# Optimization experiments

Measured on AMD Instinct MI355X. Metric: run time of the kernel, lower is better.

## Reference

```python
import jax, jax.numpy as jnp
import numpy as np

N_NODES = 100000
N_EDGES = 200000
B = 256        # batch of query (center) nodes
K = 20         # n_neighbors
D = 128        # node feature dim
TD = 128       # time encoding dim
IMP = 100      # importance_dim
DK = 256       # attention key dim
H = 4 * (D + TD)  # LSTM hidden per init_para_for_one_depth = 1024
FEAT = D + D + TD + IMP  # 484: [neigh_x, edge_x, edge_tx, neigh_imp]


def setup_inputs() -> dict:
    key = jax.random.key(0)
    ks = jax.random.split(key, 30)
    nrm = lambda k, s, sc: jax.random.normal(k, s, jnp.float32) * sc
    uni = lambda k, s: jax.random.uniform(k, s, jnp.float32)
    rint = lambda k, s, hi: jax.random.randint(k, s, 0, hi).astype(jnp.int64)
    return dict(
        node_reprs=nrm(ks[0], (N_NODES, D), 1.0),
        node_embed=nrm(ks[1], (N_NODES, D), 1.0),
        edge_embed=nrm(ks[2], (N_EDGES, D), 1.0),
        time_w=nrm(ks[3], (TD,), 1.0),
        time_b=nrm(ks[4], (TD,), 1.0),
        imp_w1=nrm(ks[5], (IMP,), 1.0),
        imp_b1=nrm(ks[6], (IMP,), 0.1),
        imp_w2=nrm(ks[7], (IMP, IMP), 1.0 / np.sqrt(IMP)),
        imp_b2=nrm(ks[8], (IMP,), 0.1),
        Wq=nrm(ks[9], (D + TD, DK), 1.0 / np.sqrt(D + TD)),
        Wk=nrm(ks[10], (FEAT, DK), 1.0 / np.sqrt(FEAT)),
        Wv=nrm(ks[11], (FEAT, DK), 1.0 / np.sqrt(FEAT)),
        lstm_wih=nrm(ks[12], (DK, 4 * H), 1.0 / np.sqrt(DK)),
        lstm_whh=nrm(ks[13], (H, 4 * H), 1.0 / np.sqrt(H)),
        lstm_b=nrm(ks[14], (4 * H,), 0.02),
        Wout=nrm(ks[15], (D + H, D), 1.0 / np.sqrt(D + H)),
        ts=uni(ks[16], (B,)),
        n2_ts=uni(ks[17], (B, K)),
        n1_ts=uni(ks[18], (B * K, K)),
        n2_re=uni(ks[19], (B, K)),
        n2_deg=uni(ks[20], (B, K)),
        n1_re=uni(ks[21], (B * K, K)),
        n1_deg=uni(ks[22], (B * K, K)),
        center_nids=rint(ks[23], (B,), N_NODES),
        n2_nids=rint(ks[24], (B, K), N_NODES),
        n2_eids=rint(ks[25], (B, K), N_EDGES),
        n1_nids=rint(ks[26], (B * K, K), N_NODES),
        n1_eids=rint(ks[27], (B * K, K), N_EDGES),
    )


def reference(node_reprs, node_embed, edge_embed, time_w, time_b,
              imp_w1, imp_b1, imp_w2, imp_b2, Wq, Wk, Wv,
              lstm_wih, lstm_whh, lstm_b, Wout,
              ts, n2_ts, n1_ts, n2_re, n2_deg, n1_re, n1_deg,
              center_nids, n2_nids, n2_eids, n1_nids, n1_eids):
    scale = jnp.asarray(1.0 / np.sqrt(DK), jnp.float32)

    def time_enc(t):
        # TimeEncode: cos(t * w + b) -> [..., TD]
        return jnp.cos(t[..., None] * time_w + time_b)

    def imp_enc(deg, re):
        # importance_score = deg / re with zero-denominator mask (masked_fill)
        safe = jnp.where(re == 0, 1.0, re)
        s = jnp.where(re == 0, 0.0, deg / safe)[..., None]  # [..., 1]
        h = jax.nn.relu(s * imp_w1 + imp_b1)
        return h @ imp_w2 + imp_b2  # [..., IMP]

    def aggregate(cx, ctx0, nx, ex, etx, mask, imp):
        # attention over K neighbors, then one LSTM-cell step on the context
        q = jnp.concatenate([cx, ctx0], -1) @ Wq                         # [n, DK]
        feat = jnp.concatenate([nx, ex, etx, imp], -1)                   # [n, K, FEAT]
        k = feat @ Wk                                                    # [n, K, DK]
        v = feat @ Wv                                                    # [n, K, DK]
        scores = jnp.einsum('nd,nkd->nk', q, k) * scale
        scores = jnp.where(mask, -1e9, scores)
        attn = jax.nn.softmax(scores, -1)
        ctx = jnp.einsum('nk,nkd->nd', attn, v)                          # [n, DK]
        h0 = jnp.zeros((cx.shape[0], H), cx.dtype)                       # init hidden = 0
        gates = ctx @ lstm_wih + h0 @ lstm_whh + lstm_b                  # [n, 4H]
        i, f, g, o = jnp.split(gates, 4, -1)
        c_new = jax.nn.sigmoid(i) * jnp.tanh(g)                          # cell init = 0 so f-term vanishes
        h_new = jax.nn.sigmoid(o) * jnp.tanh(c_new)                      # [n, H]
        return jnp.concatenate([cx, h_new], -1) @ Wout                   # [n, D]

    def node_feats(nids):
        # involved_node_reprs[local_idx] + raw node embeddings
        return node_reprs[nids] + node_embed[nids]

    # ---- depth 1 (centers = flattened level-2 neighbors) ----
    c1 = n2_nids.reshape(-1)                 # [B*K]
    ts1 = jnp.repeat(ts, K)                  # [B*K]
    cx1 = node_feats(c1)                     # [B*K, D]
    nx0 = node_feats(n1_nids)                # depth-0 base case gather [B*K, K, D]
    h1 = aggregate(cx1, time_enc(jnp.zeros_like(ts1)), nx0,
                   edge_embed[n1_eids], time_enc(ts1[:, None] - n1_ts),
                   n1_nids == 0, imp_enc(n1_deg, n1_re))                 # [B*K, D]
    h1 = h1.reshape(B, K, D)

    # ---- depth 2 (query centers) ----
    cx2 = node_feats(center_nids)            # [B, D]
    out = aggregate(cx2, time_enc(jnp.zeros_like(ts)), h1,
                    edge_embed[n2_eids], time_enc(ts[:, None] - n2_ts),
                    n2_nids == 0, imp_enc(n2_deg, n2_re))                # [B, D]
    return out
```

## Files before the change

kernel.cpp:

```cpp
#include <hip/hip_runtime.h>
#include <math.h>

#define K_NB 20
#define DIM  128
#define TDIM 128
#define IMP  100
#define DKQ  256
#define HID  1024
#define FEAT 484
#define FB   384
#define NB1  5120
#define NB2  256
#define FROW 488

__device__ __forceinline__ float sigmoidf_(float x) { return 1.f / (1.f + expf(-x)); }

__global__ __launch_bounds__(256) void precompute_k(
    const float* __restrict__ time_b, const float* __restrict__ imp_b2,
    const float* __restrict__ Wq, const float* __restrict__ Wk,
    const float* __restrict__ Wv, const float* __restrict__ W2,
    float* __restrict__ VW, float* __restrict__ WK,
    float* __restrict__ qc0, float* __restrict__ cv0)
{
    int b = blockIdx.x, t = threadIdx.x;
    if (b < FB) {
        VW[b * DKQ + t] = Wv[b * DKQ + t];
        WK[b * DKQ + t] = Wk[b * DKQ + t];
    } else if (b < FB + IMP) {
        int j = b - FB; float aV = 0.f, aK = 0.f;
        for (int m = 0; m < IMP; m++) {
            float w = W2[j * IMP + m];
            aV += w * Wv[(FB + m) * DKQ + t];
            aK += w * Wk[(FB + m) * DKQ + t];
        }
        VW[b * DKQ + t] = aV;
        WK[b * DKQ + t] = aK;
    } else if (b == FB + IMP) {
        float acc = 0.f;
        for (int j = 0; j < TDIM; j++) acc += cosf(time_b[j]) * Wq[(DIM + j) * DKQ + t];
        qc0[t] = acc;
    } else {
        float acc = 0.f;
        for (int m = 0; m < IMP; m++) acc += imp_b2[m] * Wv[(FB + m) * DKQ + t];
        cv0[t] = acc;
    }
}

__global__ __launch_bounds__(128) void precompute2_k(
    const float* __restrict__ Wq, const float* __restrict__ WK,
    const float* __restrict__ qc0, float* __restrict__ WQK, float* __restrict__ kc0)
{
    const int n = blockIdx.x, d = threadIdx.x;
    float acc = 0.f;
    for (int t = 0; t < DKQ; t++) acc += Wq[d * DKQ + t] * WK[n * DKQ + t];
    WQK[d * FEAT + n] = acc * 0.0625f;
    if (d == 0) {
        float a2 = 0.f;
        for (int t = 0; t < DKQ; t++) a2 += qc0[t] * WK[n * DKQ + t];
        kc0[n] = a2 * 0.0625f;
    }
}

__global__ __launch_bounds__(128) void cx_gather_k(
    const float* __restrict__ nr, const float* __restrict__ ne,
    const int* __restrict__ cids, float* __restrict__ CX, int nrows)
{
    int r = blockIdx.x * 4 + (threadIdx.x >> 5);
    if (r >= nrows) return;
    int c4 = (threadIdx.x & 31);
    int nid = cids[r];
    const float4 a = ((const float4*)(nr + (size_t)nid * DIM))[c4];
    const float4 b = ((const float4*)(ne + (size_t)nid * DIM))[c4];
    float4 o; o.x = a.x + b.x; o.y = a.y + b.y; o.z = a.z + b.z; o.w = a.w + b.w;
    ((float4*)(CX + (size_t)r * DIM))[c4] = o;
}

template <int BM, int BN, bool BT, int KS>
__global__ __launch_bounds__((BM / 8) * (BN / 4)) void gemm_f32(
    const float* __restrict__ A, const float* __restrict__ A2, int asplit, int lda2,
    const float* __restrict__ B, const float* __restrict__ bias,
    float* __restrict__ C, int M, int N, int K, int lda, int ldb, int ldc, float scale)
{
    constexpr int NT = (BM / 8) * (BN / 4);
    constexpr int EA = BM * 16 / NT;
    constexpr int EB = BN * 16 / NT;
    constexpr int TROW = BN / 4;
    __shared__ float As[16][BM + 4];
    __shared__ float Bs[16][BN + 4];
    const int tid = threadIdx.x;
    const int bm = blockIdx.y * BM, bn = blockIdx.x * BN;
    const int tm = (tid / TROW) * 8, tn = (tid % TROW) * 4;
    const int KCH = KS == 1 ? K : (((K + KS - 1) / KS + 15) & ~15);
    const int kbeg = blockIdx.z * KCH;
    const int kend = (kbeg + KCH < K) ? kbeg + KCH : K;
    float acc[8][4] = {};

    for (int k0 = kbeg; k0 < kend; k0 += 16) {
#pragma unroll
        for (int i = 0; i < EA; i++) {
            int flat = tid * EA + i;
            int r = flat >> 4, kc = flat & 15;
            int gk = k0 + kc;
            float v = 0.f;
            if (gk < kend) {
                int gr = bm + r;
                v = (A2 && gk >= asplit) ? A2[(size_t)gr * lda2 + (gk - asplit)]
                                         : A[(size_t)gr * lda + gk];
            }
            As[kc][r] = v;
        }
        if (!BT) {
#pragma unroll
            for (int i = 0; i < EB; i++) {
                int flat = tid * EB + i;
                int kb = flat / BN, nb = flat % BN;
                int gk = k0 + kb, gn = bn + nb;
                Bs[kb][nb] = (gk < kend && gn < N) ? B[(size_t)gk * ldb + gn] : 0.f;
            }
        } else {
#pragma unroll
            for (int i = 0; i < EB; i++) {
                int flat = tid * EB + i;
                int n = flat >> 4, kc = flat & 15;
                int gn = bn + n, gk = k0 + kc;
                Bs[kc][n] = (gn < N && gk < kend) ? B[(size_t)gn * ldb + gk] : 0.f;
            }
        }
        __syncthreads();
#pragma unroll
        for (int kk = 0; kk < 16; kk++) {
            float a[8], b[4];
#pragma unroll
            for (int i = 0; i < 8; i++) a[i] = As[kk][tm + i];
#pragma unroll
            for (int j = 0; j < 4; j++) b[j] = Bs[kk][tn + j];
#pragma unroll
            for (int i = 0; i < 8; i++)
#pragma unroll
                for (int j = 0; j < 4; j++) acc[i][j] += a[i] * b[j];
        }
        __syncthreads();
    }
#pragma unroll
    for (int i = 0; i < 8; i++) {
        int gm = bm + tm + i;
#pragma unroll
        for (int j = 0; j < 4; j++) {
            int gn = bn + tn + j;
            if (gn >= N) continue;
            float v = acc[i][j];
            if (KS == 1) {
                if (bias) v += bias[gn];
                C[(size_t)gm * ldc + gn] = v * scale;
            } else {
                if (bias && blockIdx.z == 0) v += bias[gn];
                atomicAdd(&C[(size_t)gm * ldc + gn], v * scale);
            }
        }
    }
}

template <int DEPTH>
__global__ __launch_bounds__(256) void attn_rows_k(
    const float* __restrict__ nr, const float* __restrict__ ne,
    const float* __restrict__ ee, const float* __restrict__ h1,
    const int* __restrict__ nids, const int* __restrict__ eids,
    const float* __restrict__ nts, const float* __restrict__ deg,
    const float* __restrict__ re, const float* __restrict__ ts,
    const float* __restrict__ tw, const float* __restrict__ tb,
    const float* __restrict__ iw1, const float* __restrict__ ib1,
    const float* __restrict__ KQ, float* __restrict__ WFB)
{
    __shared__ float featb[K_NB][FROW];
    __shared__ float kq_s[FROW];
    __shared__ float score[K_NB], attn_l[K_NB];
    __shared__ float dt_s[K_NB], ss_s[K_NB];
    __shared__ int nid_s[K_NB], eid_s[K_NB];

    const int row = blockIdx.x, tid = threadIdx.x;
    const int g = tid >> 5, l = tid & 31;

    if (tid < K_NB) {
        int nid = nids[row * K_NB + tid];
        nid_s[tid] = nid; eid_s[tid] = eids[row * K_NB + tid];
        float tc = (DEPTH == 1) ? ts[row / K_NB] : ts[row];
        dt_s[tid] = tc - nts[row * K_NB + tid];
        float rv = re[row * K_NB + tid];
        ss_s[tid] = (rv == 0.f) ? 0.f : deg[row * K_NB + tid] / rv;
    }
    kq_s[tid] = KQ[(size_t)row * FEAT + tid];
    if (tid < FEAT - 256) kq_s[256 + tid] = KQ[(size_t)row * FEAT + 256 + tid];
    __syncthreads();

    for (int rr = g; rr < K_NB; rr += 8) {
        const int nid = nid_s[rr], eid = eid_s[rr];
        float4 xa;
        if (DEPTH == 1) {
            const float4 a = ((const float4*)(nr + (size_t)nid * DIM))[l];
            const float4 b = ((const float4*)(ne + (size_t)nid * DIM))[l];
            xa.x = a.x + b.x; xa.y = a.y + b.y; xa.z = a.z + b.z; xa.w = a.w + b.w;
        } else {
            xa = ((const float4*)(h1 + ((size_t)row * K_NB + rr) * DIM))[l];
        }
        const float4 xe = ((const float4*)(ee + (size_t)eid * DIM))[l];
        const float dt = dt_s[rr];
        const float4 tw4 = ((const float4*)tw)[l];
        const float4 tb4 = ((const float4*)tb)[l];
        float4 xt;
        xt.x = __cosf(dt * tw4.x + tb4.x);
        xt.y = __cosf(dt * tw4.y + tb4.y);
        xt.z = __cosf(dt * tw4.z + tb4.z);
        xt.w = __cosf(dt * tw4.w + tb4.w);

        ((float4*)&featb[rr][0])[l]   = xa;
        ((float4*)&featb[rr][128])[l] = xe;
        ((float4*)&featb[rr][256])[l] = xt;

        const int c = 4 * l;
        float sc = xa.x * kq_s[c]       + xa.y * kq_s[c + 1]       + xa.z * kq_s[c + 2]       + xa.w * kq_s[c + 3]
                 + xe.x * kq_s[128 + c] + xe.y * kq_s[128 + c + 1] + xe.z * kq_s[128 + c + 2] + xe.w * kq_s[128 + c + 3]
                 + xt.x * kq_s[256 + c] + xt.y * kq_s[256 + c + 1] + xt.z * kq_s[256 + c + 2] + xt.w * kq_s[256 + c + 3];
        if (l < IMP / 4) {
            const float s = ss_s[rr];
            const float4 w1 = ((const float4*)iw1)[l];
            const float4 b1 = ((const float4*)ib1)[l];
            float4 hv;
            hv.x = fmaxf(s * w1.x + b1.x, 0.f);
            hv.y = fmaxf(s * w1.y + b1.y, 0.f);
            hv.z = fmaxf(s * w1.z + b1.z, 0.f);
            hv.w = fmaxf(s * w1.w + b1.w, 0.f);
            ((float4*)&featb[rr][FB])[l] = hv;
            sc += hv.x * kq_s[FB + c] + hv.y * kq_s[FB + c + 1]
                + hv.z * kq_s[FB + c + 2] + hv.w * kq_s[FB + c + 3];
        }
#pragma unroll
        for (int off = 16; off >= 1; off >>= 1) sc += __shfl_down(sc, off, 32);
        if (l == 0) score[rr] = sc;
    }
    __syncthreads();

    if (tid < 32) {
        float sc = (tid < K_NB) ? ((nid_s[tid] == 0) ? -1e9f : score[tid]) : -3.0e38f;
        float mx = sc;
#pragma unroll
        for (int off = 16; off >= 1; off >>= 1) mx = fmaxf(mx, __shfl_xor(mx, off, 32));
        float e = __expf(sc - mx);
        float sum = e;
#pragma unroll
        for (int off = 16; off >= 1; off >>= 1) sum += __shfl_xor(sum, off, 32);
        if (tid < K_NB) attn_l[tid] = e / sum;
    }
    __syncthreads();

    if (tid < FEAT / 4) {
        float4 acc = {0.f, 0.f, 0.f, 0.f};
#pragma unroll 4
        for (int r = 0; r < K_NB; r++) {
            const float a = attn_l[r];
            const float4 f = ((const float4*)&featb[r][0])[tid];
            acc.x += a * f.x; acc.y += a * f.y; acc.z += a * f.z; acc.w += a * f.w;
        }
        ((float4*)(WFB + (size_t)row * FEAT))[tid] = acc;
    }
}

__global__ __launch_bounds__(256) void gates_out_k(
    const float* __restrict__ CTX, const float* __restrict__ wih,
    const float* __restrict__ bias, const float* __restrict__ WoutB,
    float* __restrict__ Hout, int M)
{
    __shared__ float smem[16 * 68 + 3 * 16 * 68];
    __shared__ float Bs2[16][132];
    float* As  = smem;
    float* Bs  = smem + 16 * 68;
    float* h_s = smem;

    const int tid = threadIdx.x;
    const int bm = blockIdx.y * 64, bn = blockIdx.x * 64;
    const int tm = (tid >> 4) * 4, tn = (tid & 15) * 4;
    float acc[3][4][4] = {};

    for (int k0 = 0; k0 < DKQ; k0 += 16) {
        int r = tid >> 2, kc = (tid & 3) * 4;
#pragma unroll
        for (int i = 0; i < 4; i++) As[(kc + i) * 68 + r] = CTX[(size_t)(bm + r) * DKQ + k0 + kc + i];
        int kb = tid >> 4, nb = (tid & 15) * 4;
#pragma unroll
        for (int i = 0; i < 4; i++) {
            Bs[0 * 1088 + kb * 68 + nb + i] = wih[(size_t)(k0 + kb) * 4096 +    0 + bn + nb + i];
            Bs[1 * 1088 + kb * 68 + nb + i] = wih[(size_t)(k0 + kb) * 4096 + 2048 + bn + nb + i];
            Bs[2 * 1088 + kb * 68 + nb + i] = wih[(size_t)(k0 + kb) * 4096 + 3072 + bn + nb + i];
        }
        __syncthreads();
#pragma unroll
        for (int kk = 0; kk < 16; kk++) {
            float a[4], b0[4], b1[4], b2v[4];
#pragma unroll
            for (int i = 0; i < 4; i++) a[i] = As[kk * 68 + tm + i];
#pragma unroll
            for (int j = 0; j < 4; j++) {
                b0[j]  = Bs[0 * 1088 + kk * 68 + tn + j];
                b1[j]  = Bs[1 * 1088 + kk * 68 + tn + j];
                b2v[j] = Bs[2 * 1088 + kk * 68 + tn + j];
            }
#pragma unroll
            for (int i = 0; i < 4; i++)
#pragma unroll
                for (int j = 0; j < 4; j++) {
                    acc[0][i][j] += a[i] * b0[j];
                    acc[1][i][j] += a[i] * b1[j];
                    acc[2][i][j] += a[i] * b2v[j];
                }
        }
        __syncthreads();
    }

#pragma unroll
    for (int i = 0; i < 4; i++)
#pragma unroll
        for (int j = 0; j < 4; j++) {
            int n = bn + tn + j;
            float iv = acc[0][i][j] + bias[n];
            float gv = acc[1][i][j] + bias[2048 + n];
            float ov = acc[2][i][j] + bias[3072 + n];
            float c = sigmoidf_(iv) * tanhf(gv);
            h_s[(tm + i) * 68 + tn + j] = sigmoidf_(ov) * tanhf(c);
        }
    __syncthreads();

    const int tm2 = (tid >> 5) * 8, tn2 = (tid & 31) * 4;
    float acc2[8][4] = {};
    for (int kc0 = 0; kc0 < 64; kc0 += 16) {
#pragma unroll
        for (int i = 0; i < 8; i++) {
            int flat = tid * 8 + i;
            int kb = flat >> 7, nb = flat & 127;
            Bs2[kb][nb] = WoutB[(size_t)(bn + kc0 + kb) * DIM + nb];
        }
        __syncthreads();
#pragma unroll
        for (int kk = 0; kk < 16; kk++) {
            float a[8];
#pragma unroll
            for (int i = 0; i < 8; i++) a[i] = h_s[(tm2 + i) * 68 + kc0 + kk];
            const float4 bf = *(const float4*)&Bs2[kk][tn2];
#pragma unroll
            for (int i = 0; i < 8; i++) {
                acc2[i][0] += a[i] * bf.x; acc2[i][1] += a[i] * bf.y;
                acc2[i][2] += a[i] * bf.z; acc2[i][3] += a[i] * bf.w;
            }
        }
        __syncthreads();
    }
#pragma unroll
    for (int i = 0; i < 8; i++)
#pragma unroll
        for (int j = 0; j < 4; j++)
            atomicAdd(&Hout[(size_t)(bm + tm2 + i) * DIM + tn2 + j], acc2[i][j]);
}

extern "C" void kernel_launch(void* const* d_in, const int* in_sizes, int n_in,
                              void* d_out, int out_size, void* d_ws, size_t ws_size,
                              hipStream_t stream)
{
    const float* nr   = (const float*)d_in[0];
    const float* ne   = (const float*)d_in[1];
    const float* ee   = (const float*)d_in[2];
    const float* tw   = (const float*)d_in[3];
    const float* tb   = (const float*)d_in[4];
    const float* iw1  = (const float*)d_in[5];
    const float* ib1  = (const float*)d_in[6];
    const float* W2   = (const float*)d_in[7];
    const float* ib2  = (const float*)d_in[8];
    const float* Wq   = (const float*)d_in[9];
    const float* Wk   = (const float*)d_in[10];
    const float* Wv   = (const float*)d_in[11];
    const float* wih  = (const float*)d_in[12];
    const float* lb   = (const float*)d_in[14];
    const float* Wout = (const float*)d_in[15];
    const float* ts     = (const float*)d_in[16];
    const float* n2_ts  = (const float*)d_in[17];
    const float* n1_ts  = (const float*)d_in[18];
    const float* n2_re  = (const float*)d_in[19];
    const float* n2_deg = (const float*)d_in[20];
    const float* n1_re  = (const float*)d_in[21];
    const float* n1_deg = (const float*)d_in[22];
    const int* center_nids = (const int*)d_in[23];
    const int* n2_nids     = (const int*)d_in[24];
    const int* n2_eids     = (const int*)d_in[25];
    const int* n1_nids     = (const int*)d_in[26];
    const int* n1_eids     = (const int*)d_in[27];

    const float* WoutA = Wout;
    const float* WoutB = Wout + 128 * DIM;

    float* ws   = (float*)d_ws;
    float* VW   = ws;
    float* WK   = VW  + FEAT * DKQ;
    float* qc0  = WK  + FEAT * DKQ;
    float* cv0  = qc0 + DKQ;
    float* WQK  = cv0 + DKQ;
    float* kc0  = WQK + DIM * FEAT;
    float* CX   = kc0 + 512;
    float* H1   = CX  + NB1 * DIM;
    float* CTX  = H1  + NB1 * DIM;
    float* KQ   = CTX + NB1 * DKQ;
    float* WFB  = KQ  + NB1 * FEAT;

    precompute_k<<<FB + IMP + 2, 256, 0, stream>>>(tb, ib2, Wq, Wk, Wv, W2, VW, WK, qc0, cv0);
    precompute2_k<<<FEAT, 128, 0, stream>>>(Wq, WK, qc0, WQK, kc0);

    {
        const int M = NB1;
        cx_gather_k<<<M / 4, 128, 0, stream>>>(nr, ne, n2_nids, CX, M);
        gemm_f32<64, 64, false, 1><<<dim3(8, M / 64), 128, 0, stream>>>(
            CX, nullptr, 0, 0, WQK, kc0, KQ, M, FEAT, DIM, DIM, FEAT, FEAT, 1.f);
        attn_rows_k<1><<<M, 256, 0, stream>>>(nr, ne, ee, nullptr,
            n1_nids, n1_eids, n1_ts, n1_deg, n1_re, ts, tw, tb, iw1, ib1, KQ, WFB);
        hipMemsetAsync(CTX, 0, (size_t)M * DKQ * sizeof(float), stream);
        gemm_f32<64, 64, false, 4><<<dim3(4, M / 64, 4), 128, 0, stream>>>(
            WFB, nullptr, 0, 0, VW, cv0, CTX, M, DKQ, FEAT, FEAT, DKQ, DKQ, 1.f);
        gemm_f32<64, 32, false, 1><<<dim3(4, M / 64), 64, 0, stream>>>(
            CX, nullptr, 0, 0, WoutA, nullptr, H1, M, DIM, DIM, DIM, DIM, DIM, 1.f);
        gates_out_k<<<dim3(16, M / 64), 256, 0, stream>>>(CTX, wih, lb, WoutB, H1, M);
    }
    {
        const int M = NB2;
        cx_gather_k<<<M / 4, 128, 0, stream>>>(nr, ne, center_nids, CX, M);
        gemm_f32<64, 64, false, 1><<<dim3(8, M / 64), 128, 0, stream>>>(
            CX, nullptr, 0, 0, WQK, kc0, KQ, M, FEAT, DIM, DIM, FEAT, FEAT, 1.f);
        attn_rows_k<2><<<M, 256, 0, stream>>>(nr, ne, ee, H1,
            n2_nids, n2_eids, n2_ts, n2_deg, n2_re, ts, tw, tb, iw1, ib1, KQ, WFB);
        hipMemsetAsync(CTX, 0, (size_t)M * DKQ * sizeof(float), stream);
        gemm_f32<64, 64, false, 4><<<dim3(4, M / 64, 4), 128, 0, stream>>>(
            WFB, nullptr, 0, 0, VW, cv0, CTX, M, DKQ, FEAT, FEAT, DKQ, DKQ, 1.f);
        gemm_f32<64, 32, false, 1><<<dim3(4, M / 64), 64, 0, stream>>>(
            CX, nullptr, 0, 0, WoutA, nullptr, (float*)d_out, M, DIM, DIM, DIM, DIM, DIM, 1.f);
        gates_out_k<<<dim3(16, M / 64), 256, 0, stream>>>(CTX, wih, lb, WoutB, (float*)d_out, M);
    }
}
```

Before: 878.0 us.

## Use split-bf16 MFMA for LSTM input-gate GEMM in gates_out_k

```diff
diff --git a/kernel.cpp b/kernel.cpp
--- a/kernel.cpp
+++ b/kernel.cpp
@@ -13,7 +13,20 @@
 #define NB2  256
 #define FROW 488
 
+typedef __attribute__((ext_vector_type(8))) short short8v;
+typedef __attribute__((ext_vector_type(4))) float f32x4;
+
 __device__ __forceinline__ float sigmoidf_(float x) { return 1.f / (1.f + expf(-x)); }
+
+__device__ __forceinline__ void bfsplit(float x, unsigned short& h, unsigned short& l) {
+    unsigned u = __builtin_bit_cast(unsigned, x);
+    h = (unsigned short)(u >> 16);
+    float hi = __builtin_bit_cast(float, u & 0xFFFF0000u);
+    float r = x - hi;
+    unsigned v = __builtin_bit_cast(unsigned, r);
+    unsigned rnd = v + 0x7FFFu + ((v >> 16) & 1u);
+    l = (unsigned short)(rnd >> 16);
+}
 
 __global__ __launch_bounds__(256) void precompute_k(
     const float* __restrict__ time_b, const float* __restrict__ imp_b2,
@@ -59,6 +72,46 @@
         for (int t = 0; t < DKQ; t++) a2 += qc0[t] * WK[n * DKQ + t];
         kc0[n] = a2 * 0.0625f;
     }
+}
+
+__global__ __launch_bounds__(256) void wih_split_k(
+    const float* __restrict__ wih,
+    unsigned short* __restrict__ Th, unsigned short* __restrict__ Tl)
+{
+    __shared__ float t[64][65];
+    const int cb = blockIdx.x * 64, kb = blockIdx.y * 64;
+    const int tid = threadIdx.x;
+    {
+        int kr = tid >> 2, c0 = (tid & 3) * 16;
+#pragma unroll
+        for (int j = 0; j < 16; j++)
+            t[kr][c0 + j] = wih[(size_t)(kb + kr) * 4096 + cb + c0 + j];
+    }
+    __syncthreads();
+    {
+        int c = tid >> 2, k0 = (tid & 3) * 16;
+#pragma unroll
+        for (int j = 0; j < 16; j++) {
+            unsigned short h, l;
+            bfsplit(t[k0 + j][c], h, l);
+            Th[(size_t)(cb + c) * DKQ + kb + k0 + j] = h;
+            Tl[(size_t)(cb + c) * DKQ + kb + k0 + j] = l;
+        }
+    }
+}
+
+__global__ __launch_bounds__(256) void ctx_split_k(
+    const float* __restrict__ CTX,
+    unsigned short* __restrict__ Ch, unsigned short* __restrict__ Cl, int total4)
+{
+    int i = blockIdx.x * 256 + threadIdx.x;
+    if (i >= total4) return;
+    float4 v = ((const float4*)CTX)[i];
+    ushort4 hv, lv;
+    bfsplit(v.x, hv.x, lv.x); bfsplit(v.y, hv.y, lv.y);
+    bfsplit(v.z, hv.z, lv.z); bfsplit(v.w, hv.w, lv.w);
+    ((ushort4*)Ch)[i] = hv;
+    ((ushort4*)Cl)[i] = lv;
 }
 
 __global__ __launch_bounds__(128) void cx_gather_k(
@@ -265,67 +318,67 @@
 }
 
 __global__ __launch_bounds__(256) void gates_out_k(
-    const float* __restrict__ CTX, const float* __restrict__ wih,
+    const unsigned short* __restrict__ CTXh, const unsigned short* __restrict__ CTXl,
+    const unsigned short* __restrict__ wihTh, const unsigned short* __restrict__ wihTl,
     const float* __restrict__ bias, const float* __restrict__ WoutB,
     float* __restrict__ Hout, int M)
 {
-    __shared__ float smem[16 * 68 + 3 * 16 * 68];
+    __shared__ float h_s[64][68];
     __shared__ float Bs2[16][132];
-    float* As  = smem;
-    float* Bs  = smem + 16 * 68;
-    float* h_s = smem;
 
     const int tid = threadIdx.x;
+    const int w = tid >> 6, l = tid & 63;
+    const int lr = l & 15, lk = (l >> 4) * 8;
     const int bm = blockIdx.y * 64, bn = blockIdx.x * 64;
-    const int tm = (tid >> 4) * 4, tn = (tid & 15) * 4;
-    float acc[3][4][4] = {};
-
-    for (int k0 = 0; k0 < DKQ; k0 += 16) {
-        int r = tid >> 2, kc = (tid & 3) * 4;
-#pragma unroll
-        for (int i = 0; i < 4; i++) As[(kc + i) * 68 + r] = CTX[(size_t)(bm + r) * DKQ + k0 + kc + i];
-        int kb = tid >> 4, nb = (tid & 15) * 4;
-#pragma unroll
-        for (int i = 0; i < 4; i++) {
-            Bs[0 * 1088 + kb * 68 + nb + i] = wih[(size_t)(k0 + kb) * 4096 +    0 + bn + nb + i];
-            Bs[1 * 1088 + kb * 68 + nb + i] = wih[(size_t)(k0 + kb) * 4096 + 2048 + bn + nb + i];
-            Bs[2 * 1088 + kb * 68 + nb + i] = wih[(size_t)(k0 + kb) * 4096 + 3072 + bn + nb + i];
-        }
-        __syncthreads();
-#pragma unroll
-        for (int kk = 0; kk < 16; kk++) {
-            float a[4], b0[4], b1[4], b2v[4];
-#pragma unroll
-            for (int i = 0; i < 4; i++) a[i] = As[kk * 68 + tm + i];
-#pragma unroll
-            for (int j = 0; j < 4; j++) {
-                b0[j]  = Bs[0 * 1088 + kk * 68 + tn + j];
-                b1[j]  = Bs[1 * 1088 + kk * 68 + tn + j];
-                b2v[j] = Bs[2 * 1088 + kk * 68 + tn + j];
-            }
-#pragma unroll
-            for (int i = 0; i < 4; i++)
-#pragma unroll
-                for (int j = 0; j < 4; j++) {
-                    acc[0][i][j] += a[i] * b0[j];
-                    acc[1][i][j] += a[i] * b1[j];
-                    acc[2][i][j] += a[i] * b2v[j];
-                }
-        }
-        __syncthreads();
-    }
-
-#pragma unroll
-    for (int i = 0; i < 4; i++)
-#pragma unroll
-        for (int j = 0; j < 4; j++) {
-            int n = bn + tn + j;
-            float iv = acc[0][i][j] + bias[n];
-            float gv = acc[1][i][j] + bias[2048 + n];
-            float ov = acc[2][i][j] + bias[3072 + n];
-            float c = sigmoidf_(iv) * tanhf(gv);
-            h_s[(tm + i) * 68 + tn + j] = sigmoidf_(ov) * tanhf(c);
-        }
+
+    f32x4 acc[4][3] = {};
+    size_t arow[4];
+#pragma unroll
+    for (int m = 0; m < 4; m++) arow[m] = (size_t)(bm + 16 * m + lr) * DKQ;
+    const int goff[3] = {0, 2048, 3072};
+    size_t brow[3];
+#pragma unroll
+    for (int g = 0; g < 3; g++) brow[g] = (size_t)(goff[g] + bn + 16 * w + lr) * DKQ;
+
+    for (int k0 = 0; k0 < DKQ; k0 += 32) {
+        short8v ah[4], al[4], bh[3], bl[3];
+#pragma unroll
+        for (int m = 0; m < 4; m++) {
+            ah[m] = *(const short8v*)(CTXh + arow[m] + k0 + lk);
+            al[m] = *(const short8v*)(CTXl + arow[m] + k0 + lk);
+        }
+#pragma unroll
+        for (int g = 0; g < 3; g++) {
+            bh[g] = *(const short8v*)(wihTh + brow[g] + k0 + lk);
+            bl[g] = *(const short8v*)(wihTl + brow[g] + k0 + lk);
+        }
+#pragma unroll
+        for (int m = 0; m < 4; m++)
+#pragma unroll
+            for (int g = 0; g < 3; g++) {
+                acc[m][g] = __builtin_amdgcn_mfma_f32_16x16x32_bf16(ah[m], bh[g], acc[m][g], 0, 0, 0);
+                acc[m][g] = __builtin_amdgcn_mfma_f32_16x16x32_bf16(ah[m], bl[g], acc[m][g], 0, 0, 0);
+                acc[m][g] = __builtin_amdgcn_mfma_f32_16x16x32_bf16(al[m], bh[g], acc[m][g], 0, 0, 0);
+            }
+    }
+
+    {
+        const int col = 16 * w + lr;
+        const float bi = bias[bn + col];
+        const float bg = bias[2048 + bn + col];
+        const float bo = bias[3072 + bn + col];
+#pragma unroll
+        for (int m = 0; m < 4; m++)
+#pragma unroll
+            for (int r = 0; r < 4; r++) {
+                int row = 16 * m + (l >> 4) * 4 + r;
+                float iv = acc[m][0][r] + bi;
+                float gv = acc[m][1][r] + bg;
+                float ov = acc[m][2][r] + bo;
+                float c = sigmoidf_(iv) * tanhf(gv);
+                h_s[row][col] = sigmoidf_(ov) * tanhf(c);
+            }
+    }
     __syncthreads();
 
     const int tm2 = (tid >> 5) * 8, tn2 = (tid & 31) * 4;
@@ -342,7 +395,7 @@
         for (int kk = 0; kk < 16; kk++) {
             float a[8];
 #pragma unroll
-            for (int i = 0; i < 8; i++) a[i] = h_s[(tm2 + i) * 68 + kc0 + kk];
+            for (int i = 0; i < 8; i++) a[i] = h_s[tm2 + i][kc0 + kk];
             const float4 bf = *(const float4*)&Bs2[kk][tn2];
 #pragma unroll
             for (int i = 0; i < 8; i++) {
@@ -401,14 +454,19 @@
     float* cv0  = qc0 + DKQ;
     float* WQK  = cv0 + DKQ;
     float* kc0  = WQK + DIM * FEAT;
-    float* CX   = kc0 + 512;
+    unsigned short* wihTh = (unsigned short*)(kc0 + 512);
+    unsigned short* wihTl = wihTh + 4096 * DKQ;
+    float* CX   = (float*)(wihTl + 4096 * DKQ);
     float* H1   = CX  + NB1 * DIM;
     float* CTX  = H1  + NB1 * DIM;
     float* KQ   = CTX + NB1 * DKQ;
     float* WFB  = KQ  + NB1 * FEAT;
+    unsigned short* CTXh = (unsigned short*)KQ;
+    unsigned short* CTXl = CTXh + NB1 * DKQ;
 
     precompute_k<<<FB + IMP + 2, 256, 0, stream>>>(tb, ib2, Wq, Wk, Wv, W2, VW, WK, qc0, cv0);
     precompute2_k<<<FEAT, 128, 0, stream>>>(Wq, WK, qc0, WQK, kc0);
+    wih_split_k<<<dim3(4096 / 64, DKQ / 64), 256, 0, stream>>>(wih, wihTh, wihTl);
 
     {
         const int M = NB1;
@@ -420,9 +478,11 @@
         hipMemsetAsync(CTX, 0, (size_t)M * DKQ * sizeof(float), stream);
         gemm_f32<64, 64, false, 4><<<dim3(4, M / 64, 4), 128, 0, stream>>>(
             WFB, nullptr, 0, 0, VW, cv0, CTX, M, DKQ, FEAT, FEAT, DKQ, DKQ, 1.f);
+        ctx_split_k<<<(M * DKQ / 4 + 255) / 256, 256, 0, stream>>>(CTX, CTXh, CTXl, M * DKQ / 4);
         gemm_f32<64, 32, false, 1><<<dim3(4, M / 64), 64, 0, stream>>>(
             CX, nullptr, 0, 0, WoutA, nullptr, H1, M, DIM, DIM, DIM, DIM, DIM, 1.f);
-        gates_out_k<<<dim3(16, M / 64), 256, 0, stream>>>(CTX, wih, lb, WoutB, H1, M);
+        gates_out_k<<<dim3(16, M / 64), 256, 0, stream>>>(
+            CTXh, CTXl, wihTh, wihTl, lb, WoutB, H1, M);
     }
     {
         const int M = NB2;
@@ -434,8 +494,10 @@
         hipMemsetAsync(CTX, 0, (size_t)M * DKQ * sizeof(float), stream);
         gemm_f32<64, 64, false, 4><<<dim3(4, M / 64, 4), 128, 0, stream>>>(
             WFB, nullptr, 0, 0, VW, cv0, CTX, M, DKQ, FEAT, FEAT, DKQ, DKQ, 1.f);
+        ctx_split_k<<<(M * DKQ / 4 + 255) / 256, 256, 0, stream>>>(CTX, CTXh, CTXl, M * DKQ / 4);
         gemm_f32<64, 32, false, 1><<<dim3(4, M / 64), 64, 0, stream>>>(
             CX, nullptr, 0, 0, WoutA, nullptr, (float*)d_out, M, DIM, DIM, DIM, DIM, DIM, 1.f);
-        gates_out_k<<<dim3(16, M / 64), 256, 0, stream>>>(CTX, wih, lb, WoutB, (float*)d_out, M);
-    }
-}
+        gates_out_k<<<dim3(16, M / 64), 256, 0, stream>>>(
+            CTXh, CTXl, wihTh, wihTl, lb, WoutB, (float*)d_out, M);
+    }
+}
```

Result: slower. 917.2 us (+4.5%).
